# Kernel optimization log

Hardware: AMD Instinct MI355X
Metric: run time of the kernel (lower is better)

The kernel has to match this reference:

```python
import jax, jax.numpy as jnp
import numpy as np

MU = 5
ITERATIONS = 3


def _sobel(x):
    # torch kernel: stack([K, K.T]) with K = vertical-gradient Sobel; conv2d is cross-correlation
    k = jnp.array([[-1., -2., -1.], [0., 0., 0.], [1., 2., 1.]], dtype=x.dtype)
    kern = jnp.stack([k, k.T])[:, None]  # [2,1,3,3] -> channels (Gy, Gx)
    return jax.lax.conv_general_dilated(
        x, kern, window_strides=(1, 1), padding=[(1, 1), (1, 1)],
        dimension_numbers=("NCHW", "OIHW", "NCHW"))


def _normalize(v):
    # norm over channel dim, zeros replaced by 1 (matches tang_mag[tang_mag==0]=1)
    mag = jnp.linalg.norm(v, axis=1, keepdims=True)
    mag = jnp.where(mag == 0, jnp.ones_like(mag), mag)
    return v / mag


def etf_forward(inputs, mu=MU, iterations=ITERATIONS):
    B, _, H, W = inputs.shape
    sobel = _sobel(inputs)                                   # [B,2,H,W]
    sobel_mag = jnp.linalg.norm(sobel, axis=1, keepdims=True)
    sobel_mag = sobel_mag / jnp.max(sobel_mag)               # [B,1,H,W]
    pad = lambda t: jnp.pad(t, ((0, 0), (0, 0), (mu, mu), (mu, mu)))
    sobel_mag_padded = pad(sobel_mag)
    sobel_X = sobel_mag
    # tang = sobel.flip(channels) * [-1, 1] => [-Gx, Gy], then normalized
    tang = jnp.stack([-sobel[:, 1], sobel[:, 0]], axis=1)
    tang = _normalize(tang)
    for _ in range(iterations):
        for ori in ("Vertical", "Horizontal"):
            tang_padded = pad(tang)
            tang_X = tang
            acc = jnp.zeros_like(tang)
            for i in range(2 * mu + 1):
                if ori == "Vertical":
                    tang_Y = tang_padded[:, :, i:i + H, mu:mu + W]
                    sobel_Y = sobel_mag_padded[:, :, i:i + H, mu:mu + W]
                else:
                    tang_Y = tang_padded[:, :, mu:mu + H, i:i + W]
                    sobel_Y = sobel_mag_padded[:, :, mu:mu + H, i:i + W]
                w = (jnp.tanh(sobel_Y - sobel_X) + 1.0) * jnp.sum(tang_X * tang_Y, axis=1, keepdims=True) * 0.5
                acc = acc + tang_Y * w
            tang = _normalize(acc)
    return tang


def setup_inputs() -> dict:
    key = jax.random.key(0)
    inputs = jax.random.uniform(key, (2, 1, 1024, 1024), dtype=jnp.float32)
    return {"inputs": inputs}


def reference(inputs) -> jnp.ndarray:
    return etf_forward(inputs)
```

## Files before the change

### kernel.cpp

```cpp
#include <hip/hip_runtime.h>

#define BB 2
#define HH 1024
#define WW 1024
#define MU 5

#define TH 32
#define TW 64
#define SH (TH + 2 * MU)
#define SCW 80
#define SMS 83
#define SVS 81

__device__ __forceinline__ float fast_rcp(float x) { return __builtin_amdgcn_rcpf(x); }
__device__ __forceinline__ float fast_rsq(float x) { return __builtin_amdgcn_rsqf(x); }

#define SR 8
__global__ __launch_bounds__(256) void sobel_init(
    const float* __restrict__ x,
    float* __restrict__ tf,
    float* __restrict__ mag,
    float* __restrict__ block_max)
{
    __shared__ float xs[SR + 2][264];
    const int t = threadIdx.x;
    const int w0 = blockIdx.x * 256;
    const int h0 = blockIdx.y * SR;
    const int b = blockIdx.z;
    const size_t plane = (size_t)HH * WW;
    const float* xb = x + (size_t)b * plane;

    for (int i = t; i < (SR + 2) * 66; i += 256) {
        int r = i / 66, c4 = i % 66;
        int g = h0 - 1 + r;
        int gw = w0 - 4 + 4 * c4;
        float4 v = make_float4(0.f, 0.f, 0.f, 0.f);
        if (g >= 0 && g < HH && gw >= 0 && gw < WW)
            v = *(const float4*)(xb + (size_t)g * WW + gw);
        *(float4*)&xs[r][4 * c4] = v;
    }
    __syncthreads();

    float lmax = 0.f;
    const int c = 4 + t;
    #pragma unroll
    for (int k = 0; k < SR; ++k) {
        const float* rT = xs[k], * rM = xs[k + 1], * rB = xs[k + 2];
        float tl = rT[c - 1], tc = rT[c], tr = rT[c + 1];
        float ml = rM[c - 1],             mr = rM[c + 1];
        float bl = rB[c - 1], bc = rB[c], br = rB[c + 1];
        float s0 = (bl - tl) + 2.f * (bc - tc) + (br - tr);
        float s1 = (tr - tl) + 2.f * (mr - ml) + (br - bl);
        float m = sqrtf(fmaf(s0, s0, s1 * s1));
        float inv = (m == 0.f) ? 1.f : fast_rcp(m);
        size_t gi = (size_t)(h0 + k) * WW + (w0 + t);
        mag[(size_t)b * plane + gi] = m;
        ((float2*)tf)[(size_t)b * plane + gi] = make_float2(-s1 * inv, s0 * inv);
        lmax = fmaxf(lmax, m);
    }

    #pragma unroll
    for (int off = 32; off; off >>= 1) lmax = fmaxf(lmax, __shfl_down(lmax, off, 64));
    __shared__ float smax[4];
    if ((t & 63) == 0) smax[t >> 6] = lmax;
    __syncthreads();
    if (t == 0)
        block_max[(blockIdx.z * 128 + blockIdx.y) * 4 + blockIdx.x] =
            fmaxf(fmaxf(smax[0], smax[1]), fmaxf(smax[2], smax[3]));
}

__global__ __launch_bounds__(256) void reduce_max(
    const float* __restrict__ block_max, float* __restrict__ gmax)
{
    const int t = threadIdx.x;
    float m = 0.f;
    #pragma unroll
    for (int i = 0; i < 4; ++i) m = fmaxf(m, block_max[t + 256 * i]);
    #pragma unroll
    for (int off = 32; off; off >>= 1) m = fmaxf(m, __shfl_down(m, off, 64));
    __shared__ float smax[4];
    if ((t & 63) == 0) smax[t >> 6] = m;
    __syncthreads();
    if (t == 0) gmax[0] = fmaxf(fmaxf(smax[0], smax[1]), fmaxf(smax[2], smax[3]));
}

template <int PLANAR_OUT>
__global__ __launch_bounds__(256, 4) void etf_vh(
    const float* __restrict__ tin,
    float* __restrict__ tout,
    const float* __restrict__ mag,
    const float* __restrict__ gmax)
{
    __shared__ float lds[SH * SCW * 2 + SH * SMS];
    float* st  = lds;
    float* sm  = lds + SH * SCW * 2;
    float* sv0 = lds;
    float* sv1 = lds + TH * SVS;

    const int t = threadIdx.x;
    const int w0 = blockIdx.x * TW;
    const int h0 = blockIdx.y * TH;
    const int b = blockIdx.z;
    const size_t plane = (size_t)HH * WW;
    const float* tb = tin + 2 * (size_t)b * plane;
    const float* mb = mag + (size_t)b * plane;
    const float s2 = 2.f * fast_rcp(gmax[0]);

    for (int i = t; i < SH * 40 + SH * 20; i += 256) {
        if (i < SH * 40) {
            int r = i / 40, c4 = i % 40;
            int g = h0 - MU + r;
            int gw = w0 - 8 + 2 * c4;
            float4 v = make_float4(0.f, 0.f, 0.f, 0.f);
            if (g >= 0 && g < HH && gw >= 0 && gw < WW)
                v = *(const float4*)(tb + 2 * ((size_t)g * WW + gw));
            *(float4*)&st[r * (SCW * 2) + 4 * c4] = v;
        } else {
            int j = i - SH * 40;
            int r = j / 20, c4 = j % 20;
            int g = h0 - MU + r;
            int gw = w0 - 8 + 4 * c4;
            float4 v = make_float4(0.f, 0.f, 0.f, 0.f);
            if (g >= 0 && g < HH && gw >= 0 && gw < WW)
                v = *(const float4*)(mb + (size_t)g * WW + gw);
            float* dst = &sm[r * SMS + 4 * c4];
            dst[0] = __expf(-s2 * v.x);
            dst[1] = __expf(-s2 * v.y);
            dst[2] = __expf(-s2 * v.z);
            dst[3] = __expf(-s2 * v.w);
        }
    }
    __syncthreads();

    float r0a[21], r1a[21], rea[21];

    const int c = t % 80;
    const int strip = t / 80;
    const int vr0row = strip * 11;
    const int Rv = (strip == 2) ? 10 : 11;
    if (t < 240) {
        #pragma unroll
        for (int j = 0; j < 21; ++j) {
            if (j < Rv + 10) {
                float2 v = *(const float2*)&st[((vr0row + j) * SCW + c) * 2];
                r0a[j] = v.x; r1a[j] = v.y;
                rea[j] = sm[(vr0row + j) * SMS + c];
            }
        }
    }
    __syncthreads();

    if (t < 240) {
        #pragma unroll
        for (int i = 0; i < 11; ++i) {
            if (i < Rv) {
                float tx0 = r0a[i + 5], tx1 = r1a[i + 5];
                float remx = fast_rcp(rea[i + 5]);
                float a0 = 0.f, a1 = 0.f;
                #pragma unroll
                for (int d = 0; d <= 2 * MU; ++d) {
                    float y0 = r0a[i + d], y1 = r1a[i + d], ey = rea[i + d];
                    float s = fast_rcp(fmaf(ey, remx, 1.f));
                    float w = s * fmaf(tx0, y0, tx1 * y1);
                    a0 = fmaf(y0, w, a0);
                    a1 = fmaf(y1, w, a1);
                }
                float n2 = fmaf(a0, a0, a1 * a1);
                float inv = (n2 == 0.f) ? 1.f : fast_rsq(n2);
                sv0[(vr0row + i) * SVS + c] = a0 * inv;
                sv1[(vr0row + i) * SVS + c] = a1 * inv;
            }
        }
    }
    __syncthreads();

    const int r = t & 31;
    const int cg = t >> 5;
    const int cbase = 8 + cg * 8;
    #pragma unroll
    for (int j = 0; j < 18; ++j) {
        int sc = cbase - 5 + j;
        r0a[j] = sv0[r * SVS + sc];
        r1a[j] = sv1[r * SVS + sc];
        rea[j] = sm[(r + MU) * SMS + sc];
    }
    __syncthreads();

    #pragma unroll
    for (int k = 0; k < 8; ++k) {
        float tx0 = r0a[k + 5], tx1 = r1a[k + 5];
        float remx = fast_rcp(rea[k + 5]);
        float a0 = 0.f, a1 = 0.f;
        #pragma unroll
        for (int d = 0; d <= 2 * MU; ++d) {
            float y0 = r0a[k + d], y1 = r1a[k + d], ey = rea[k + d];
            float s = fast_rcp(fmaf(ey, remx, 1.f));
            float w = s * fmaf(tx0, y0, tx1 * y1);
            a0 = fmaf(y0, w, a0);
            a1 = fmaf(y1, w, a1);
        }
        float n2 = fmaf(a0, a0, a1 * a1);
        float inv = (n2 == 0.f) ? 1.f : fast_rsq(n2);
        sv0[r * SVS + cbase + k] = a0 * inv;
        sv1[r * SVS + cbase + k] = a1 * inv;
    }
    __syncthreads();

    #pragma unroll
    for (int m = 0; m < 8; ++m) {
        int px = t + 256 * m;
        int rr = px >> 6, cc = px & 63;
        float v0 = sv0[rr * SVS + 8 + cc];
        float v1 = sv1[rr * SVS + 8 + cc];
        size_t gi = (size_t)(h0 + rr) * WW + (w0 + cc);
        if (PLANAR_OUT) {
            tout[(size_t)(2 * b)     * plane + gi] = v0;
            tout[(size_t)(2 * b + 1) * plane + gi] = v1;
        } else {
            *(float2*)&tout[2 * ((size_t)b * plane + gi)] = make_float2(v0, v1);
        }
    }
}

extern "C" void kernel_launch(void* const* d_in, const int* in_sizes, int n_in,
                              void* d_out, int out_size, void* d_ws, size_t ws_size,
                              hipStream_t stream)
{
    const float* x = (const float*)d_in[0];
    char* ws = (char*)d_ws;
    const size_t plane = (size_t)HH * WW;

    float* tfA  = (float*)ws;
    float* tfB  = (float*)(ws + sizeof(float) * BB * 2 * plane);
    float* mag  = (float*)(ws + sizeof(float) * BB * 4 * plane);
    float* gmax = (float*)(ws + sizeof(float) * BB * 6 * plane);
    float* block_max = gmax + 16;

    sobel_init<<<dim3(4, 128, BB), 256, 0, stream>>>(x, tfA, mag, block_max);
    reduce_max<<<1, 256, 0, stream>>>(block_max, gmax);

    dim3 g(WW / TW, HH / TH, BB);
    etf_vh<0><<<g, 256, 0, stream>>>(tfA, tfB, mag, gmax);
    etf_vh<0><<<g, 256, 0, stream>>>(tfB, tfA, mag, gmax);
    etf_vh<1><<<g, 256, 0, stream>>>(tfA, (float*)d_out, mag, gmax);
}
```

Baseline: 131.7 us.

## Fuse max reduction into sobel via last-block atomic, write outputs directly

Removes the separate reduce_max launch: each sobel block publishes its max, increments an atomic counter, and the last block finishes the global max reduction. That costs a hipMemsetAsync per call to reset the counter. The horizontal pass now writes results straight to global memory instead of staging them through LDS, which drops two syncthreads and the final copy loop, but the stores are less coalesced. The workspace layout moves gmax to a new offset.

Measured after the change: 170.1 us. +29.1%, slower.

```diff
diff --git a/kernel.cpp b/kernel.cpp
--- a/kernel.cpp
+++ b/kernel.cpp
@@ -18,15 +18,18 @@
 #define SR 8
 __global__ __launch_bounds__(256) void sobel_init(
     const float* __restrict__ x,
-    float* __restrict__ tf,
+    float2* __restrict__ tf,
     float* __restrict__ mag,
-    float* __restrict__ block_max)
+    float* __restrict__ block_max,
+    unsigned int* __restrict__ counter,
+    float* __restrict__ gmax)
 {
     __shared__ float xs[SR + 2][264];
     const int t = threadIdx.x;
     const int w0 = blockIdx.x * 256;
     const int h0 = blockIdx.y * SR;
     const int b = blockIdx.z;
+    const int bid = (blockIdx.z * 128 + blockIdx.y) * 4 + blockIdx.x;
     const size_t plane = (size_t)HH * WW;
     const float* xb = x + (size_t)b * plane;
 
@@ -55,38 +58,38 @@
         float inv = (m == 0.f) ? 1.f : fast_rcp(m);
         size_t gi = (size_t)(h0 + k) * WW + (w0 + t);
         mag[(size_t)b * plane + gi] = m;
-        ((float2*)tf)[(size_t)b * plane + gi] = make_float2(-s1 * inv, s0 * inv);
+        tf[(size_t)b * plane + gi] = make_float2(-s1 * inv, s0 * inv);
         lmax = fmaxf(lmax, m);
     }
 
     #pragma unroll
     for (int off = 32; off; off >>= 1) lmax = fmaxf(lmax, __shfl_down(lmax, off, 64));
     __shared__ float smax[4];
+    __shared__ int lastflag;
     if ((t & 63) == 0) smax[t >> 6] = lmax;
     __syncthreads();
-    if (t == 0)
-        block_max[(blockIdx.z * 128 + blockIdx.y) * 4 + blockIdx.x] =
-            fmaxf(fmaxf(smax[0], smax[1]), fmaxf(smax[2], smax[3]));
-}
-
-__global__ __launch_bounds__(256) void reduce_max(
-    const float* __restrict__ block_max, float* __restrict__ gmax)
-{
-    const int t = threadIdx.x;
-    float m = 0.f;
-    #pragma unroll
-    for (int i = 0; i < 4; ++i) m = fmaxf(m, block_max[t + 256 * i]);
-    #pragma unroll
-    for (int off = 32; off; off >>= 1) m = fmaxf(m, __shfl_down(m, off, 64));
-    __shared__ float smax[4];
-    if ((t & 63) == 0) smax[t >> 6] = m;
-    __syncthreads();
-    if (t == 0) gmax[0] = fmaxf(fmaxf(smax[0], smax[1]), fmaxf(smax[2], smax[3]));
+    if (t == 0) {
+        block_max[bid] = fmaxf(fmaxf(smax[0], smax[1]), fmaxf(smax[2], smax[3]));
+        __threadfence();
+        unsigned int old = atomicAdd(counter, 1u);
+        lastflag = (old == 1023u);
+    }
+    __syncthreads();
+    if (lastflag) {
+        __threadfence();
+        float m = fmaxf(fmaxf(block_max[t], block_max[t + 256]),
+                        fmaxf(block_max[t + 512], block_max[t + 768]));
+        #pragma unroll
+        for (int off = 32; off; off >>= 1) m = fmaxf(m, __shfl_down(m, off, 64));
+        if ((t & 63) == 0) smax[t >> 6] = m;
+        __syncthreads();
+        if (t == 0) gmax[0] = fmaxf(fmaxf(smax[0], smax[1]), fmaxf(smax[2], smax[3]));
+    }
 }
 
 template <int PLANAR_OUT>
 __global__ __launch_bounds__(256, 4) void etf_vh(
-    const float* __restrict__ tin,
+    const float2* __restrict__ tin,
     float* __restrict__ tout,
     const float* __restrict__ mag,
     const float* __restrict__ gmax)
@@ -102,8 +105,8 @@
     const int h0 = blockIdx.y * TH;
     const int b = blockIdx.z;
     const size_t plane = (size_t)HH * WW;
-    const float* tb = tin + 2 * (size_t)b * plane;
-    const float* mb = mag + (size_t)b * plane;
+    const float2* tb = tin + (size_t)b * plane;
+    const float*  mb = mag + (size_t)b * plane;
     const float s2 = 2.f * fast_rcp(gmax[0]);
 
     for (int i = t; i < SH * 40 + SH * 20; i += 256) {
@@ -113,7 +116,7 @@
             int gw = w0 - 8 + 2 * c4;
             float4 v = make_float4(0.f, 0.f, 0.f, 0.f);
             if (g >= 0 && g < HH && gw >= 0 && gw < WW)
-                v = *(const float4*)(tb + 2 * ((size_t)g * WW + gw));
+                v = *(const float4*)(tb + (size_t)g * WW + gw);
             *(float4*)&st[r * (SCW * 2) + 4 * c4] = v;
         } else {
             int j = i - SH * 40;
@@ -134,17 +137,17 @@
 
     float r0a[21], r1a[21], rea[21];
 
-    const int c = t % 80;
+    const int vc = t % 80;
     const int strip = t / 80;
-    const int vr0row = strip * 11;
+    const int vrow = strip * 11;
     const int Rv = (strip == 2) ? 10 : 11;
     if (t < 240) {
         #pragma unroll
         for (int j = 0; j < 21; ++j) {
             if (j < Rv + 10) {
-                float2 v = *(const float2*)&st[((vr0row + j) * SCW + c) * 2];
+                float2 v = *(const float2*)&st[((vrow + j) * SCW + vc) * 2];
                 r0a[j] = v.x; r1a[j] = v.y;
-                rea[j] = sm[(vr0row + j) * SMS + c];
+                rea[j] = sm[(vrow + j) * SMS + vc];
             }
         }
     }
@@ -159,33 +162,29 @@
                 float a0 = 0.f, a1 = 0.f;
                 #pragma unroll
                 for (int d = 0; d <= 2 * MU; ++d) {
-                    float y0 = r0a[i + d], y1 = r1a[i + d], ey = rea[i + d];
-                    float s = fast_rcp(fmaf(ey, remx, 1.f));
-                    float w = s * fmaf(tx0, y0, tx1 * y1);
-                    a0 = fmaf(y0, w, a0);
-                    a1 = fmaf(y1, w, a1);
+                    float s = fast_rcp(fmaf(rea[i + d], remx, 1.f));
+                    float w = s * fmaf(tx0, r0a[i + d], tx1 * r1a[i + d]);
+                    a0 = fmaf(r0a[i + d], w, a0);
+                    a1 = fmaf(r1a[i + d], w, a1);
                 }
                 float n2 = fmaf(a0, a0, a1 * a1);
                 float inv = (n2 == 0.f) ? 1.f : fast_rsq(n2);
-                sv0[(vr0row + i) * SVS + c] = a0 * inv;
-                sv1[(vr0row + i) * SVS + c] = a1 * inv;
+                sv0[(vrow + i) * SVS + vc] = a0 * inv;
+                sv1[(vrow + i) * SVS + vc] = a1 * inv;
             }
         }
     }
     __syncthreads();
 
-    const int r = t & 31;
+    const int r  = t & 31;
     const int cg = t >> 5;
-    const int cbase = 8 + cg * 8;
+    const int cb = 8 + cg * 8;
     #pragma unroll
     for (int j = 0; j < 18; ++j) {
-        int sc = cbase - 5 + j;
-        r0a[j] = sv0[r * SVS + sc];
-        r1a[j] = sv1[r * SVS + sc];
-        rea[j] = sm[(r + MU) * SMS + sc];
-    }
-    __syncthreads();
-
+        r0a[j] = sv0[r * SVS + cb - MU + j];
+        r1a[j] = sv1[r * SVS + cb - MU + j];
+        rea[j] = sm[(r + MU) * SMS + cb - MU + j];
+    }
     #pragma unroll
     for (int k = 0; k < 8; ++k) {
         float tx0 = r0a[k + 5], tx1 = r1a[k + 5];
@@ -193,31 +192,19 @@
         float a0 = 0.f, a1 = 0.f;
         #pragma unroll
         for (int d = 0; d <= 2 * MU; ++d) {
-            float y0 = r0a[k + d], y1 = r1a[k + d], ey = rea[k + d];
-            float s = fast_rcp(fmaf(ey, remx, 1.f));
-            float w = s * fmaf(tx0, y0, tx1 * y1);
-            a0 = fmaf(y0, w, a0);
-            a1 = fmaf(y1, w, a1);
+            float s = fast_rcp(fmaf(rea[k + d], remx, 1.f));
+            float w = s * fmaf(tx0, r0a[k + d], tx1 * r1a[k + d]);
+            a0 = fmaf(r0a[k + d], w, a0);
+            a1 = fmaf(r1a[k + d], w, a1);
         }
         float n2 = fmaf(a0, a0, a1 * a1);
         float inv = (n2 == 0.f) ? 1.f : fast_rsq(n2);
-        sv0[r * SVS + cbase + k] = a0 * inv;
-        sv1[r * SVS + cbase + k] = a1 * inv;
-    }
-    __syncthreads();
-
-    #pragma unroll
-    for (int m = 0; m < 8; ++m) {
-        int px = t + 256 * m;
-        int rr = px >> 6, cc = px & 63;
-        float v0 = sv0[rr * SVS + 8 + cc];
-        float v1 = sv1[rr * SVS + 8 + cc];
-        size_t gi = (size_t)(h0 + rr) * WW + (w0 + cc);
+        size_t gi = (size_t)(h0 + r) * WW + (w0 + cg * 8 + k);
         if (PLANAR_OUT) {
-            tout[(size_t)(2 * b)     * plane + gi] = v0;
-            tout[(size_t)(2 * b + 1) * plane + gi] = v1;
+            tout[(size_t)(2 * b)     * plane + gi] = a0 * inv;
+            tout[(size_t)(2 * b + 1) * plane + gi] = a1 * inv;
         } else {
-            *(float2*)&tout[2 * ((size_t)b * plane + gi)] = make_float2(v0, v1);
+            ((float2*)tout)[(size_t)b * plane + gi] = make_float2(a0 * inv, a1 * inv);
         }
     }
 }
@@ -230,17 +217,20 @@
     char* ws = (char*)d_ws;
     const size_t plane = (size_t)HH * WW;
 
-    float* tfA  = (float*)ws;
-    float* tfB  = (float*)(ws + sizeof(float) * BB * 2 * plane);
+    float2* tfA = (float2*)ws;
+    float2* tfB = (float2*)(ws + sizeof(float) * BB * 2 * plane);
     float* mag  = (float*)(ws + sizeof(float) * BB * 4 * plane);
-    float* gmax = (float*)(ws + sizeof(float) * BB * 6 * plane);
+    float* gmax = (float*)(ws + sizeof(float) * BB * 5 * plane);
     float* block_max = gmax + 16;
-
-    sobel_init<<<dim3(4, 128, BB), 256, 0, stream>>>(x, tfA, mag, block_max);
-    reduce_max<<<1, 256, 0, stream>>>(block_max, gmax);
+    unsigned int* counter = (unsigned int*)(block_max + 1024);
+
+    hipMemsetAsync(counter, 0, sizeof(unsigned int), stream);
+
+    sobel_init<<<dim3(4, 128, BB), 256, 0, stream>>>(x, tfA, mag, block_max,
+                                                     counter, gmax);
 
     dim3 g(WW / TW, HH / TH, BB);
-    etf_vh<0><<<g, 256, 0, stream>>>(tfA, tfB, mag, gmax);
-    etf_vh<0><<<g, 256, 0, stream>>>(tfB, tfA, mag, gmax);
+    etf_vh<0><<<g, 256, 0, stream>>>(tfA, (float*)tfB, mag, gmax);
+    etf_vh<0><<<g, 256, 0, stream>>>(tfB, (float*)tfA, mag, gmax);
     etf_vh<1><<<g, 256, 0, stream>>>(tfA, (float*)d_out, mag, gmax);
 }
```
